# Optimization experiments

Measured on AMD Instinct MI355X. Metric: run time of the kernel, lower is better.

## Reference

```python
import jax, jax.numpy as jnp
import numpy as np

B, N, E = 32, 2048, 4096
D_IN, C, H = 256, 64, 4          # node_hidden_size, gnn_hidden_size, num_heads
SLOPE = 0.2                       # PyG GATConv default negative_slope


def gat_conv(x, src, dst, W, att_src, att_dst, bias):
    """One PyG-style GATConv (concat=True, add_self_loops=True) on a single graph.
    x: [N, Din]; src/dst: [E] int; W: [Din, H*C]; att_*: [H, C]; bias: [H*C]."""
    n = x.shape[0]
    h = (x @ W).reshape(n, H, C)                       # [N,H,C]
    a_src = jnp.einsum('nhc,hc->nh', h, att_src)       # [N,H]
    a_dst = jnp.einsum('nhc,hc->nh', h, att_dst)
    loop = jnp.arange(n, dtype=src.dtype)              # self loops
    s = jnp.concatenate([src, loop])
    d = jnp.concatenate([dst, loop])
    e = jax.nn.leaky_relu(a_src[s] + a_dst[d], SLOPE)  # [E+N,H]
    # segment softmax over incoming edges of each target node
    m = jax.ops.segment_max(e, d, num_segments=n)
    ex = jnp.exp(e - m[d])
    denom = jax.ops.segment_sum(ex, d, num_segments=n)
    alpha = ex / (denom[d] + 1e-16)                    # [E+N,H]
    out = jax.ops.segment_sum(alpha[:, :, None] * h[s], d, num_segments=n)  # [N,H,C]
    return out.reshape(n, H * C) + bias


def setup_inputs() -> dict:
    key = jax.random.key(0)
    ks = jax.random.split(key, 12)
    g = lambda k, shp, fan: jax.random.normal(k, shp, jnp.float32) * (1.0 / np.sqrt(fan))
    return {
        'node_embeddings': jax.random.normal(ks[0], (B, N, D_IN), jnp.float32),
        'src_index': jax.random.randint(ks[1], (B, E), 0, N, jnp.int32),
        'tgt_index': jax.random.randint(ks[2], (B, E), 0, N, jnp.int32),
        'W1': g(ks[3], (D_IN, H * C), D_IN),
        'att_src1': g(ks[4], (H, C), C),
        'att_dst1': g(ks[5], (H, C), C),
        'bias1': jnp.zeros((H * C,), jnp.float32),
        'W2': g(ks[6], (H * C, H * C), H * C),
        'att_src2': g(ks[7], (H, C), C),
        'att_dst2': g(ks[8], (H, C), C),
        'bias2': jnp.zeros((H * C,), jnp.float32),
    }


def reference(node_embeddings, src_index, tgt_index, W1, att_src1, att_dst1, bias1,
              W2, att_src2, att_dst2, bias2):
    def per_graph(x, s, d):
        m = gat_conv(x, s, d, W1, att_src1, att_dst1, bias1)
        m = jax.nn.elu(m)                              # dropout = identity (eval)
        m = gat_conv(m, s, d, W2, att_src2, att_dst2, bias2)
        return m
    return jax.vmap(per_graph)(node_embeddings, src_index, tgt_index)  # [B,N,H*C]
```

## Files before the change

kernel.cpp:

```cpp
#include <hip/hip_runtime.h>
#include <hip/hip_bf16.h>
#include <cstdint>

#define BB 32
#define NN 2048
#define EE 4096
#define HH 4
#define CC 64
#define DD 256
#define MM (BB*NN)

typedef __attribute__((ext_vector_type(8))) short bf16x8;
typedef __attribute__((ext_vector_type(8))) unsigned short u16x8;
typedef __attribute__((ext_vector_type(4))) float f32x4;

__device__ __forceinline__ float b2f(__hip_bfloat16 x){ return __bfloat162float(x); }
__device__ __forceinline__ float u2f(unsigned short u){ return __uint_as_float((unsigned)u << 16); }
__device__ __forceinline__ unsigned short f2u(float f){
  __hip_bfloat16 h = __float2bfloat16(f);
  return *(unsigned short*)&h;
}
__device__ __forceinline__ float ldany(const void* p, int isf, size_t i){
  return isf ? ((const float*)p)[i] : b2f(((const __hip_bfloat16*)p)[i]);
}
__device__ __forceinline__ void gld_lds16(const void* g, void* l){
  __builtin_amdgcn_global_load_lds((const __attribute__((address_space(1))) uint32_t*)g,
                                   (__attribute__((address_space(3))) uint32_t*)l, 16, 0, 0);
}

__global__ void detect_kernel(const unsigned* __restrict__ w, int* __restrict__ flag){
  __shared__ int cnt;
  if(threadIdx.x == 0) cnt = 0;
  __syncthreads();
  int c = 0;
  #pragma unroll
  for(int i = 0; i < 4; ++i){
    unsigned v = w[threadIdx.x*4 + i];
    unsigned elo = (v >> 7) & 0xFFu;
    if(elo >= 100u && elo <= 150u) ++c;
  }
  atomicAdd(&cnt, c);
  __syncthreads();
  if(threadIdx.x == 0) *flag = (cnt < 128) ? 1 : 0;
}

__global__ __launch_bounds__(256) void prep_kernel(const void* __restrict__ W1,
    const void* __restrict__ W2, __hip_bfloat16* __restrict__ W1t,
    __hip_bfloat16* __restrict__ W2t,
    const void* s0, const void* s1, const void* s2, const void* s3,
    const void* s4, const void* s5, float* __restrict__ attf,
    int* __restrict__ degc, const int* __restrict__ flag)
{
  int isf = *flag;
  int bid = blockIdx.x, t = threadIdx.x;
  if(bid < 512){
    const void* W = (bid < 256) ? W1 : W2;
    __hip_bfloat16* WT = (bid < 256) ? W1t : W2t;
    int i = (bid & 255)*256 + t;
    WT[i] = __float2bfloat16(ldany(W, isf, (size_t)(i & 255)*256 + (i >> 8)));
  } else if(bid < 518){
    int i = (bid - 512)*256 + t;
    int seg = i >> 8, off = i & 255;
    const void* s = seg==0?s0 : seg==1?s1 : seg==2?s2 : seg==3?s3 : seg==4?s4 : s5;
    attf[i] = ldany(s, isf, off);
  } else {
    int i = (bid - 518)*256 + t;
    int4 z = {0,0,0,0};
    *((int4*)degc + i) = z;
  }
}

template<int DYNA>
__global__ __launch_bounds__(256, 4) void mfma_gemm(const void* __restrict__ Ap,
    const __hip_bfloat16* __restrict__ BT, __hip_bfloat16* __restrict__ C,
    const float* __restrict__ attS, const float* __restrict__ attD,
    float* __restrict__ aS, float* __restrict__ aD, const int* __restrict__ flag)
{
  __shared__ __align__(16) short lds[16384];
  const int isf  = DYNA ? *flag : 0;
  const int tid  = threadIdx.x;
  const int w    = tid >> 6, lane = tid & 63;
  const int dd   = blockIdx.x;
  const int xcd  = dd & 7, slot = dd >> 3;
  const int rb   = xcd*64 + (slot >> 1), cb = slot & 1;
  const int row0 = rb*128, col0 = cb*128;
  const int wr   = (w & 1)*64, wc = (w >> 1)*64;
  const int fm   = lane & 15, quad = lane >> 4;
  const int srow = lane >> 2;
  const int sslot= lane & 3;
  f32x4 acc[4][4] = {};

  const float* Af = (const float*)Ap;
  const short* Ab = (const short*)Ap;
  const int fr = tid >> 1;
  const int fh = tid & 1;
  float4 fa0, fa1, fa2, fa3;

  auto stageB = [&](int t, int cur){
    short* lB = lds + cur*8192 + 4096;
    #pragma unroll
    for(int c = 0; c < 2; ++c){
      int rB = w*32 + c*16 + srow;
      const short* gb = (const short*)BT + (size_t)(col0 + rB)*DD + t*32
                        + ((sslot ^ ((rB ^ (rB >> 3)) & 3))*8);
      gld_lds16(gb, lB + (w*32 + c*16)*32);
    }
  };
  auto stageA16 = [&](int t, int cur){
    short* lA = lds + cur*8192;
    #pragma unroll
    for(int c = 0; c < 2; ++c){
      int rA = w*32 + c*16 + srow;
      const short* ga = Ab + (size_t)(row0 + rA)*DD + t*32
                        + ((sslot ^ ((rA ^ (rA >> 3)) & 3))*8);
      gld_lds16(ga, lA + (w*32 + c*16)*32);
    }
  };
  auto loadA32 = [&](int t){
    const float* p = Af + (size_t)(row0 + fr)*DD + t*32 + fh*16;
    fa0 = ((const float4*)p)[0]; fa1 = ((const float4*)p)[1];
    fa2 = ((const float4*)p)[2]; fa3 = ((const float4*)p)[3];
  };
  auto writeA32 = [&](int cur){
    short* lA = lds + cur*8192;
    int sg = (fr ^ (fr >> 3)) & 3;
    u16x8 o0, o1;
    o0[0]=f2u(fa0.x); o0[1]=f2u(fa0.y); o0[2]=f2u(fa0.z); o0[3]=f2u(fa0.w);
    o0[4]=f2u(fa1.x); o0[5]=f2u(fa1.y); o0[6]=f2u(fa1.z); o0[7]=f2u(fa1.w);
    o1[0]=f2u(fa2.x); o1[1]=f2u(fa2.y); o1[2]=f2u(fa2.z); o1[3]=f2u(fa2.w);
    o1[4]=f2u(fa3.x); o1[5]=f2u(fa3.y); o1[6]=f2u(fa3.z); o1[7]=f2u(fa3.w);
    *(u16x8*)(lA + fr*32 + (((2*fh  ) ^ sg)*8)) = o0;
    *(u16x8*)(lA + fr*32 + (((2*fh+1) ^ sg)*8)) = o1;
  };

  if(DYNA && isf){ loadA32(0); writeA32(0); }
  else           { stageA16(0, 0); }
  stageB(0, 0);
  __syncthreads();

  #pragma unroll 2
  for(int t = 0; t < 8; ++t){
    const int cur = t & 1, nxt = cur ^ 1;
    const bool pre = (t < 7);
    if(pre){
      if(DYNA && isf) loadA32(t+1);
      else            stageA16(t+1, nxt);
      stageB(t+1, nxt);
    }
    {
      const short* lA = lds + cur*8192;
      const short* lB = lds + cur*8192 + 4096;
      bf16x8 af[4], bfv[4];
      #pragma unroll
      for(int i = 0; i < 4; ++i){
        int m = wr + i*16 + fm;
        af[i]  = *(const bf16x8*)&lA[m*32 + ((quad ^ ((m ^ (m >> 3)) & 3))*8)];
        int n = wc + i*16 + fm;
        bfv[i] = *(const bf16x8*)&lB[n*32 + ((quad ^ ((n ^ (n >> 3)) & 3))*8)];
      }
      #pragma unroll
      for(int i = 0; i < 4; ++i)
        #pragma unroll
        for(int j = 0; j < 4; ++j)
          acc[i][j] = __builtin_amdgcn_mfma_f32_16x16x32_bf16(af[i], bfv[j], acc[i][j], 0, 0, 0);
    }
    if(pre && DYNA && isf) writeA32(nxt);
    __syncthreads();
  }

  const int headI = (col0 + wc) >> 6;
  float ws_[4], wd_[4];
  #pragma unroll
  for(int j = 0; j < 4; ++j){
    ws_[j] = attS[headI*CC + j*16 + fm];
    wd_[j] = attD[headI*CC + j*16 + fm];
  }
  #pragma unroll
  for(int i = 0; i < 4; ++i){
    #pragma unroll
    for(int r = 0; r < 4; ++r){
      float s = 0.f, dv = 0.f;
      #pragma unroll
      for(int j = 0; j < 4; ++j){
        float v = acc[i][j][r];
        s  += v * ws_[j];
        dv += v * wd_[j];
      }
      #pragma unroll
      for(int m = 1; m <= 8; m <<= 1){
        s  += __shfl_xor(s,  m);
        dv += __shfl_xor(dv, m);
      }
      if(fm == i*4 + r){
        int row = row0 + wr + i*16 + quad*4 + r;
        aS[(size_t)row*HH + headI] = s;
        aD[(size_t)row*HH + headI] = dv;
      }
    }
  }

  #pragma unroll
  for(int i = 0; i < 4; ++i)
    #pragma unroll
    for(int j = 0; j < 4; ++j)
      #pragma unroll
      for(int r = 0; r < 4; ++r){
        int rl = wr + i*16 + quad*4 + r;
        int cl = wc + j*16 + fm;
        lds[rl*128 + (cl ^ ((rl & 12) << 2))] = (short)f2u(acc[i][j][r]);
      }
  __syncthreads();
  const int rr = tid >> 4, cc = (tid & 15)*8;
  #pragma unroll
  for(int p = 0; p < 8; ++p){
    int rl = p*16 + rr;
    u16x8 v = *(const u16x8*)&lds[rl*128 + (cc ^ ((rl & 12) << 2))];
    *(u16x8*)((unsigned short*)C + (size_t)(row0 + rl)*DD + col0 + cc) = v;
  }
}

__global__ __launch_bounds__(256) void deg_kernel(const int* __restrict__ dst, int* __restrict__ degc)
{
  int idx = blockIdx.x*256 + threadIdx.x;
  if(idx >= BB*EE) return;
  int b = idx >> 12;
  atomicAdd(&degc[b*NN + dst[idx]], 1);
}

__global__ __launch_bounds__(256) void scan_kernel(int* __restrict__ degc, int* __restrict__ row_ptr)
{
  __shared__ int part[256];
  int b = blockIdx.x, t = threadIdx.x;
  int loc[8], s = 0;
  #pragma unroll
  for(int i = 0; i < 8; ++i){ loc[i] = s; s += degc[b*NN + t*8 + i]; }
  part[t] = s;
  __syncthreads();
  if(t == 0){
    int run = 0;
    for(int i = 0; i < 256; ++i){ int tmp = part[i]; part[i] = run; run += tmp; }
  }
  __syncthreads();
  int base = b*EE + part[t];
  #pragma unroll
  for(int i = 0; i < 8; ++i){
    int v = base + loc[i];
    row_ptr[b*(NN+1) + t*8 + i] = v;
    degc   [b*NN     + t*8 + i] = v;
  }
  if(t == 255) row_ptr[b*(NN+1) + NN] = base + s;
}

__global__ __launch_bounds__(256) void scatter_kernel(const int* __restrict__ src,
    const int* __restrict__ dst, int* __restrict__ cursor, unsigned short* __restrict__ srcList)
{
  int idx = blockIdx.x*256 + threadIdx.x;
  if(idx >= BB*EE) return;
  int b = idx >> 12;
  int pos = atomicAdd(&cursor[b*NN + dst[idx]], 1);
  srcList[pos] = (unsigned short)src[idx];
}

template<int LAYER>
__global__ __launch_bounds__(256) void gather_kernel(const __hip_bfloat16* __restrict__ H,
    const float* __restrict__ a_src, const float* __restrict__ a_dst,
    const int* __restrict__ row_ptr, const unsigned short* __restrict__ srcList,
    const float* __restrict__ bias, void* __restrict__ outp,
    const int* __restrict__ flag)
{
  int blk  = blockIdx.x;
  int vblk = (blk & 7)*2048 + (blk >> 3);
  int wid  = vblk*4 + (int)(threadIdx.x >> 6);
  int lane = threadIdx.x & 63;
  int b = wid >> 11, d = wid & (NN-1);
  int head = lane >> 4;
  int start = row_ptr[b*(NN+1) + d];
  int end   = row_ptr[b*(NN+1) + d + 1];
  const unsigned short* Hu = (const unsigned short*)H;

  float adv = a_dst[wid*HH + head];
  float sv  = a_src[wid*HH + head] + adv;
  sv = sv > 0.f ? sv : 0.2f*sv;
  float exs = __expf(sv);

  ushort4 hv = *(const ushort4*)(Hu + (size_t)wid*DD + lane*4);
  f32x4 acc;
  acc.x = exs*u2f(hv.x); acc.y = exs*u2f(hv.y); acc.z = exs*u2f(hv.z); acc.w = exs*u2f(hv.w);
  float den = exs;

  int e = start;
  float ax = 0.f; ushort4 hw = {0,0,0,0};
  if(e < end){
    int s = srcList[e];
    ax = a_src[(b*NN + s)*HH + head];
    hw = *(const ushort4*)(Hu + (size_t)(b*NN + s)*DD + lane*4);
  }
  while(e < end){
    float axn = 0.f; ushort4 hwn = {0,0,0,0};
    if(e + 1 < end){
      int sn = srcList[e+1];
      axn = a_src[(b*NN + sn)*HH + head];
      hwn = *(const ushort4*)(Hu + (size_t)(b*NN + sn)*DD + lane*4);
    }
    float v = ax + adv;
    v = v > 0.f ? v : 0.2f*v;
    float ex = __expf(v);
    acc.x += ex*u2f(hw.x); acc.y += ex*u2f(hw.y); acc.z += ex*u2f(hw.z); acc.w += ex*u2f(hw.w);
    den += ex;
    ax = axn; hw = hwn; ++e;
  }
  float inv = 1.f / (den + 1e-16f);
  float4 bs = *(const float4*)(bias + lane*4);
  float o0 = acc.x*inv + bs.x, o1 = acc.y*inv + bs.y;
  float o2 = acc.z*inv + bs.z, o3 = acc.w*inv + bs.w;
  size_t oi = (size_t)wid*DD + lane*4;
  if(LAYER == 1){
    o0 = o0 > 0.f ? o0 : expm1f(o0);
    o1 = o1 > 0.f ? o1 : expm1f(o1);
    o2 = o2 > 0.f ? o2 : expm1f(o2);
    o3 = o3 > 0.f ? o3 : expm1f(o3);
    ushort4 ov = { f2u(o0), f2u(o1), f2u(o2), f2u(o3) };
    *(ushort4*)((unsigned short*)outp + oi) = ov;
  } else {
    if(*flag){
      float4 ov = { o0, o1, o2, o3 };
      *(float4*)((float*)outp + oi) = ov;
    } else {
      ushort4 ov = { f2u(o0), f2u(o1), f2u(o2), f2u(o3) };
      *(ushort4*)((unsigned short*)outp + oi) = ov;
    }
  }
}

extern "C" void kernel_launch(void* const* d_in, const int* in_sizes, int n_in,
                              void* d_out, int out_size, void* d_ws, size_t ws_size,
                              hipStream_t stream)
{
  const void* x_in = d_in[0];
  const int*  srcI = (const int*)d_in[1];
  const int*  dstI = (const int*)d_in[2];
  const void* W1   = d_in[3];
  const void* as1  = d_in[4];
  const void* ad1  = d_in[5];
  const void* b1   = d_in[6];
  const void* W2   = d_in[7];
  const void* as2  = d_in[8];
  const void* ad2  = d_in[9];
  const void* b2   = d_in[10];

  char* ws = (char*)d_ws;
  __hip_bfloat16* R1  = (__hip_bfloat16*)ws; ws += (size_t)MM*DD*2;
  __hip_bfloat16* R2  = (__hip_bfloat16*)ws; ws += (size_t)MM*DD*2;
  float* a_src = (float*)ws; ws += (size_t)MM*HH*4;
  float* a_dst = (float*)ws; ws += (size_t)MM*HH*4;
  __hip_bfloat16* W1t = (__hip_bfloat16*)ws; ws += (size_t)DD*DD*2;
  __hip_bfloat16* W2t = (__hip_bfloat16*)ws; ws += (size_t)DD*DD*2;
  float* attf = (float*)ws; ws += 1536*4;
  int*   degc = (int*)ws;   ws += (size_t)BB*NN*4;
  int*   rowp = (int*)ws;   ws += (size_t)BB*(NN+1)*4;
  unsigned short* srcL = (unsigned short*)ws; ws += (size_t)BB*EE*2;
  int*   flag = (int*)ws;   ws += 8;

  const int gemmBlocks   = (MM/128)*(DD/128);
  const int edgeBlocks   = (BB*EE)/256;
  const int gatherBlocks = (MM*64)/256;

  detect_kernel<<<1, 64, 0, stream>>>((const unsigned*)x_in, flag);
  prep_kernel<<<582, 256, 0, stream>>>(W1, W2, W1t, W2t,
                                       as1, ad1, b1, as2, ad2, b2, attf, degc, flag);

  deg_kernel    <<<edgeBlocks, 256, 0, stream>>>(dstI, degc);
  scan_kernel   <<<BB,         256, 0, stream>>>(degc, rowp);
  scatter_kernel<<<edgeBlocks, 256, 0, stream>>>(srcI, dstI, degc, srcL);

  mfma_gemm<1><<<gemmBlocks, 256, 0, stream>>>(x_in, W1t, R2, attf + 0, attf + 256,
                                               a_src, a_dst, flag);
  gather_kernel<1><<<gatherBlocks, 256, 0, stream>>>(R2, a_src, a_dst, rowp, srcL,
                                                     attf + 512, R1, flag);
  mfma_gemm<0><<<gemmBlocks, 256, 0, stream>>>(R1, W2t, R2, attf + 768, attf + 1024,
                                               a_src, a_dst, flag);
  gather_kernel<2><<<gatherBlocks, 256, 0, stream>>>(R2, a_src, a_dst, rowp, srcL,
                                                     attf + 1280, d_out, flag);
}
```

Baseline: 245.4 us.

## Pre-convert fp32 input to bf16 and triple-buffer GEMM with async LDS loads

```diff
diff --git a/kernel.cpp b/kernel.cpp
--- a/kernel.cpp
+++ b/kernel.cpp
@@ -70,14 +70,25 @@
   }
 }
 
+__global__ __launch_bounds__(256) void convX_kernel(const float* __restrict__ src,
+    unsigned short* __restrict__ dst, const int* __restrict__ flag){
+  if(!*flag) return;
+  int blk  = blockIdx.x;
+  int vblk = (blk & 7)*2048 + (blk >> 3);
+  size_t i = ((size_t)vblk*256 + threadIdx.x)*4;
+  float4 v = *(const float4*)(src + i);
+  ushort4 o = { f2u(v.x), f2u(v.y), f2u(v.z), f2u(v.w) };
+  *(ushort4*)(dst + i) = o;
+}
+
 template<int DYNA>
-__global__ __launch_bounds__(256, 4) void mfma_gemm(const void* __restrict__ Ap,
-    const __hip_bfloat16* __restrict__ BT, __hip_bfloat16* __restrict__ C,
+__global__ __launch_bounds__(256, 3) void mfma_gemm(const __hip_bfloat16* __restrict__ A0,
+    const __hip_bfloat16* __restrict__ A1, const __hip_bfloat16* __restrict__ BT,
+    __hip_bfloat16* __restrict__ C,
     const float* __restrict__ attS, const float* __restrict__ attD,
     float* __restrict__ aS, float* __restrict__ aD, const int* __restrict__ flag)
 {
-  __shared__ __align__(16) short lds[16384];
-  const int isf  = DYNA ? *flag : 0;
+  __shared__ __align__(16) short lds[24576];
   const int tid  = threadIdx.x;
   const int w    = tid >> 6, lane = tid & 63;
   const int dd   = blockIdx.x;
@@ -86,87 +97,13 @@
   const int row0 = rb*128, col0 = cb*128;
   const int wr   = (w & 1)*64, wc = (w >> 1)*64;
   const int fm   = lane & 15, quad = lane >> 4;
-  const int srow = lane >> 2;
-  const int sslot= lane & 3;
-  f32x4 acc[4][4] = {};
-
-  const float* Af = (const float*)Ap;
-  const short* Ab = (const short*)Ap;
-  const int fr = tid >> 1;
-  const int fh = tid & 1;
-  float4 fa0, fa1, fa2, fa3;
-
-  auto stageB = [&](int t, int cur){
-    short* lB = lds + cur*8192 + 4096;
-    #pragma unroll
-    for(int c = 0; c < 2; ++c){
-      int rB = w*32 + c*16 + srow;
-      const short* gb = (const short*)BT + (size_t)(col0 + rB)*DD + t*32
-                        + ((sslot ^ ((rB ^ (rB >> 3)) & 3))*8);
-      gld_lds16(gb, lB + (w*32 + c*16)*32);
-    }
-  };
-  auto stageA16 = [&](int t, int cur){
-    short* lA = lds + cur*8192;
-    #pragma unroll
-    for(int c = 0; c < 2; ++c){
-      int rA = w*32 + c*16 + srow;
-      const short* ga = Ab + (size_t)(row0 + rA)*DD + t*32
-                        + ((sslot ^ ((rA ^ (rA >> 3)) & 3))*8);
-      gld_lds16(ga, lA + (w*32 + c*16)*32);
-    }
-  };
-  auto loadA32 = [&](int t){
-    const float* p = Af + (size_t)(row0 + fr)*DD + t*32 + fh*16;
-    fa0 = ((const float4*)p)[0]; fa1 = ((const float4*)p)[1];
-    fa2 = ((const float4*)p)[2]; fa3 = ((const float4*)p)[3];
-  };
-  auto writeA32 = [&](int cur){
-    short* lA = lds + cur*8192;
-    int sg = (fr ^ (fr >> 3)) & 3;
-    u16x8 o0, o1;
-    o0[0]=f2u(fa0.x); o0[1]=f2u(fa0.y); o0[2]=f2u(fa0.z); o0[3]=f2u(fa0.w);
-    o0[4]=f2u(fa1.x); o0[5]=f2u(fa1.y); o0[6]=f2u(fa1.z); o0[7]=f2u(fa1.w);
-    o1[0]=f2u(fa2.x); o1[1]=f2u(fa2.y); o1[2]=f2u(fa2.z); o1[3]=f2u(fa2.w);
-    o1[4]=f2u(fa3.x); o1[5]=f2u(fa3.y); o1[6]=f2u(fa3.z); o1[7]=f2u(fa3.w);
-    *(u16x8*)(lA + fr*32 + (((2*fh  ) ^ sg)*8)) = o0;
-    *(u16x8*)(lA + fr*32 + (((2*fh+1) ^ sg)*8)) = o1;
-  };
-
-  if(DYNA && isf){ loadA32(0); writeA32(0); }
-  else           { stageA16(0, 0); }
-  stageB(0, 0);
-  __syncthreads();
-
-  #pragma unroll 2
-  for(int t = 0; t < 8; ++t){
-    const int cur = t & 1, nxt = cur ^ 1;
-    const bool pre = (t < 7);
-    if(pre){
-      if(DYNA && isf) loadA32(t+1);
-      else            stageA16(t+1, nxt);
-      stageB(t+1, nxt);
-    }
-    {
-      const short* lA = lds + cur*8192;
-      const short* lB = lds + cur*8192 + 4096;
-      bf16x8 af[4], bfv[4];
-      #pragma unroll
-      for(int i = 0; i < 4; ++i){
-        int m = wr + i*16 + fm;
-        af[i]  = *(const bf16x8*)&lA[m*32 + ((quad ^ ((m ^ (m >> 3)) & 3))*8)];
-        int n = wc + i*16 + fm;
-        bfv[i] = *(const bf16x8*)&lB[n*32 + ((quad ^ ((n ^ (n >> 3)) & 3))*8)];
-      }
-      #pragma unroll
-      for(int i = 0; i < 4; ++i)
-        #pragma unroll
-        for(int j = 0; j < 4; ++j)
-          acc[i][j] = __builtin_amdgcn_mfma_f32_16x16x32_bf16(af[i], bfv[j], acc[i][j], 0, 0, 0);
-    }
-    if(pre && DYNA && isf) writeA32(nxt);
-    __syncthreads();
-  }
+  const short* Ab = (const short*)A0;
+  if(DYNA && *flag) Ab = (const short*)A1;
+  const short* Bb = (const short*)BT;
+
+  const int jof   = lane >> 3;
+  const int rpar  = (lane >> 2) & 1;
+  const int lslot = lane & 3;
 
   const int headI = (col0 + wc) >> 6;
   float ws_[4], wd_[4];
@@ -175,6 +112,60 @@
     ws_[j] = attS[headI*CC + j*16 + fm];
     wd_[j] = attD[headI*CC + j*16 + fm];
   }
+
+  f32x4 acc[4][4] = {};
+
+  auto stage = [&](int t, short* buf){
+    #pragma unroll
+    for(int c = 0; c < 2; ++c){
+      int j = w*16 + c*8 + jof;
+      int s = lslot ^ (j & 3);
+      const short* ga = Ab + (size_t)(row0 + 2*j + rpar)*DD + t*32 + s*8;
+      gld_lds16(ga, buf + (w*16 + c*8)*64);
+    }
+    #pragma unroll
+    for(int c = 0; c < 2; ++c){
+      int j = w*16 + c*8 + jof;
+      int s = lslot ^ (j & 3);
+      const short* gb = Bb + (size_t)(col0 + 2*j + rpar)*DD + t*32 + s*8;
+      gld_lds16(gb, buf + 4096 + (w*16 + c*8)*64);
+    }
+  };
+  auto compute = [&](const short* buf){
+    const short* lA = buf;
+    const short* lB = buf + 4096;
+    bf16x8 af[4], bfv[4];
+    #pragma unroll
+    for(int i = 0; i < 4; ++i){
+      int m = wr + i*16 + fm;
+      af[i]  = *(const bf16x8*)&lA[(m >> 1)*64 + (((m & 1)*4 + (quad ^ ((m >> 1) & 3)))*8)];
+      int n = wc + i*16 + fm;
+      bfv[i] = *(const bf16x8*)&lB[(n >> 1)*64 + (((n & 1)*4 + (quad ^ ((n >> 1) & 3)))*8)];
+    }
+    #pragma unroll
+    for(int i = 0; i < 4; ++i)
+      #pragma unroll
+      for(int j = 0; j < 4; ++j)
+        acc[i][j] = __builtin_amdgcn_mfma_f32_16x16x32_bf16(af[i], bfv[j], acc[i][j], 0, 0, 0);
+  };
+
+  stage(0, lds);
+  stage(1, lds + 8192);
+  asm volatile("s_waitcnt vmcnt(4)" ::: "memory");
+  __builtin_amdgcn_sched_barrier(0);
+  __builtin_amdgcn_s_barrier();
+  #pragma unroll
+  for(int t = 0; t < 8; ++t){
+    if(t < 6) stage(t + 2, lds + ((t + 2) % 3)*8192);
+    compute(lds + (t % 3)*8192);
+    if(t < 6) asm volatile("s_waitcnt vmcnt(4)" ::: "memory");
+    else      asm volatile("s_waitcnt vmcnt(0)" ::: "memory");
+    __builtin_amdgcn_sched_barrier(0);
+    asm volatile("s_waitcnt lgkmcnt(0)" ::: "memory");
+    __builtin_amdgcn_sched_barrier(0);
+    __builtin_amdgcn_s_barrier();
+  }
+
   #pragma unroll
   for(int i = 0; i < 4; ++i){
     #pragma unroll
@@ -368,17 +359,19 @@
   detect_kernel<<<1, 64, 0, stream>>>((const unsigned*)x_in, flag);
   prep_kernel<<<582, 256, 0, stream>>>(W1, W2, W1t, W2t,
                                        as1, ad1, b1, as2, ad2, b2, attf, degc, flag);
+  convX_kernel<<<(int)(((size_t)MM*DD)/1024), 256, 0, stream>>>((const float*)x_in,
+                                       (unsigned short*)R1, flag);
 
   deg_kernel    <<<edgeBlocks, 256, 0, stream>>>(dstI, degc);
   scan_kernel   <<<BB,         256, 0, stream>>>(degc, rowp);
   scatter_kernel<<<edgeBlocks, 256, 0, stream>>>(srcI, dstI, degc, srcL);
 
-  mfma_gemm<1><<<gemmBlocks, 256, 0, stream>>>(x_in, W1t, R2, attf + 0, attf + 256,
-                                               a_src, a_dst, flag);
+  mfma_gemm<1><<<gemmBlocks, 256, 0, stream>>>((const __hip_bfloat16*)x_in, R1, W1t, R2,
+                                               attf + 0, attf + 256, a_src, a_dst, flag);
   gather_kernel<1><<<gatherBlocks, 256, 0, stream>>>(R2, a_src, a_dst, rowp, srcL,
                                                      attf + 512, R1, flag);
-  mfma_gemm<0><<<gemmBlocks, 256, 0, stream>>>(R1, W2t, R2, attf + 768, attf + 1024,
-                                               a_src, a_dst, flag);
+  mfma_gemm<0><<<gemmBlocks, 256, 0, stream>>>(R1, nullptr, W2t, R2,
+                                               attf + 768, attf + 1024, a_src, a_dst, flag);
   gather_kernel<2><<<gatherBlocks, 256, 0, stream>>>(R2, a_src, a_dst, rowp, srcL,
                                                      attf + 1280, d_out, flag);
 }
```

Result: no change. 245.8 us (+0.2%).
